# Kernel tuning notes

Hardware: AMD Instinct MI355X
Metric: run time of the kernel (lower is better)

Reference implementation:

```python
import jax, jax.numpy as jnp
from jax import lax
import numpy as np

BINS = 25
K = 5  # entropy patch size
EPS = 1e-5


def conv2d(x, w, b, stride, pad):
    y = lax.conv_general_dilated(x, w, (stride, stride), [(pad, pad), (pad, pad)],
                                 dimension_numbers=("NCHW", "OIHW", "NCHW"))
    return y + b[None, :, None, None]


def group_norm_per_channel(x, w, b):
    # GroupNorm with num_groups == num_channels: per-channel norm over H,W (biased var)
    mu = x.mean(axis=(2, 3), keepdims=True)
    v = x.var(axis=(2, 3), keepdims=True)
    return (x - mu) / jnp.sqrt(v + EPS) * w[None, :, None, None] + b[None, :, None, None]


def channel_entropy(x):
    # x: (b,c,h,w). Unfold into 5x5 patches, per-patch histc(bins=25) over patch
    # values using that patch's min/max range (torch.histc default), then entropy.
    b, c, h, w = x.shape
    ho, wo = h - K + 1, w - K + 1
    # (b,c,K*K,L) -- fixed 25-position loop, vectorized over all data dims
    patches = jnp.stack([x[:, :, i:i + ho, j:j + wo]
                         for i in range(K) for j in range(K)], axis=2)
    patches = patches.reshape(b, c, K * K, ho * wo)
    mn = patches.min(axis=2, keepdims=True)
    mx = patches.max(axis=2, keepdims=True)
    rng = jnp.where(mx > mn, mx - mn, jnp.ones_like(mx))
    bins = jnp.clip(jnp.floor((patches - mn) / rng * BINS), 0, BINS - 1).astype(jnp.int32)
    # histogram via comparison one-hot: (b,c,L,BINS)
    counts = (bins[..., None] == jnp.arange(BINS, dtype=jnp.int32)).sum(axis=2)
    pk = counts.astype(x.dtype) / (K * K)
    ent = (-pk * jnp.log(jnp.clip(pk, 1e-5, 1.0 - 1e-5))).sum(axis=-1).mean(axis=-1)  # (b,c)
    return ent[:, :, None, None]


def instance_norm_ent(x, w, b):
    ent = channel_entropy(lax.stop_gradient(x))
    mu = x.mean(axis=(2, 3), keepdims=True)
    n = x.shape[2] * x.shape[3]
    v = x.var(axis=(2, 3), keepdims=True) * (n / (n - 1))  # unbiased var (torch default)
    return (x - mu) / jnp.sqrt(v + EPS) * w[None, :, None, None] * ent + b[None, :, None, None]


def setup_inputs() -> dict:
    key = jax.random.key(0)
    ks = jax.random.split(key, 24)
    s = 0.05
    d = {
        "x": jax.random.normal(ks[0], (64, 3, 224, 224), jnp.float32),
        "conv0_w": jax.random.normal(ks[1], (8, 3, 7, 7), jnp.float32) * s,
        "conv0_b": jax.random.normal(ks[2], (8,), jnp.float32) * s,
        "conv1_w": jax.random.normal(ks[3], (16, 8, 5, 5), jnp.float32) * s,
        "conv1_b": jax.random.normal(ks[4], (16,), jnp.float32) * s,
        "conv2_w": jax.random.normal(ks[5], (32, 16, 3, 3), jnp.float32) * s,
        "conv2_b": jax.random.normal(ks[6], (32,), jnp.float32) * s,
        "gn0_w": jnp.ones((8,), jnp.float32) + jax.random.normal(ks[7], (8,), jnp.float32) * s,
        "gn0_b": jax.random.normal(ks[8], (8,), jnp.float32) * s,
        "n1_w": jnp.ones((16,), jnp.float32) + jax.random.normal(ks[9], (16,), jnp.float32) * s,
        "n1_b": jax.random.normal(ks[10], (16,), jnp.float32) * s,
        "n2_w": jnp.ones((32,), jnp.float32) + jax.random.normal(ks[11], (32,), jnp.float32) * s,
        "n2_b": jax.random.normal(ks[12], (32,), jnp.float32) * s,
        "bn_g": jnp.ones((10368,), jnp.float32) + jax.random.normal(ks[13], (10368,), jnp.float32) * s,
        "bn_b": jax.random.normal(ks[14], (10368,), jnp.float32) * s,
        "fc1_w": jax.random.normal(ks[15], (32, 10368), jnp.float32) * 0.01,
        "fc1_b": jax.random.normal(ks[16], (32,), jnp.float32) * s,
        "shape_w": jax.random.normal(ks[17], (5, 32), jnp.float32) * s,
        "shape_b": jax.random.normal(ks[18], (5,), jnp.float32) * s,
        "vern_w": jax.random.normal(ks[19], (2, 32), jnp.float32) * s,
        "vern_b": jax.random.normal(ks[20], (2,), jnp.float32) * s,
    }
    return d


def reference(x, conv0_w, conv0_b, conv1_w, conv1_b, conv2_w, conv2_b,
              gn0_w, gn0_b, n1_w, n1_b, n2_w, n2_b,
              bn_g, bn_b, fc1_w, fc1_b, shape_w, shape_b, vern_w, vern_b):
    h = conv2d(x, conv0_w, conv0_b, 4, 2)          # (b,8,56,56)
    h = jax.nn.relu(group_norm_per_channel(h, gn0_w, gn0_b))
    h = conv2d(h, conv1_w, conv1_b, 3, 1)          # (b,16,18,18)
    h = jax.nn.relu(instance_norm_ent(h, n1_w, n1_b))
    h = conv2d(h, conv2_w, conv2_b, 1, 1)          # (b,32,18,18)
    h = jax.nn.relu(instance_norm_ent(h, n2_w, n2_b))
    h = h.reshape(h.shape[0], -1)                  # (b,10368)
    # BatchNorm1d (training mode: batch stats, biased var)
    mu = h.mean(axis=0)
    v = h.var(axis=0)
    h = (h - mu) / jnp.sqrt(v + EPS) * bn_g + bn_b
    h = jax.nn.relu(h @ fc1_w.T + fc1_b)           # (b,32)
    out_shape = jax.nn.softmax(h @ shape_w.T + shape_b, axis=-1)
    out_vern = jax.nn.softmax(h @ vern_w.T + vern_b, axis=-1)
    return (out_shape, out_vern)
```

## Files before the change

kernel.cpp:

```cpp
#include <hip/hip_runtime.h>
#include <math.h>

#define EPSD 1e-5


__device__ __forceinline__ double waveReduceSumD(double v) {
#pragma unroll
    for (int off = 32; off > 0; off >>= 1)
        v += __shfl_down(v, off, 64);
    return v;
}

template <int NW>
__device__ __forceinline__ double blockReduceSumD(double v, double* buf) {
    int lane = threadIdx.x & 63;
    int w = threadIdx.x >> 6;
    v = waveReduceSumD(v);
    __syncthreads();
    if (lane == 0) buf[w] = v;
    __syncthreads();
    double tot = 0.0;
#pragma unroll
    for (int i = 0; i < NW; i++) tot += buf[i];
    return tot;
}

__device__ __forceinline__ void build_ent_tab(float* tab) {
    int t = threadIdx.x;
    if (t < 26) {
        if (t == 0) tab[0] = 0.f;
        else {
            double pk = (double)t / 25.0;
            double cl = fmin(fmax(pk, 1e-5), 1.0 - 1e-5);
            tab[t] = (float)(-pk * log(cl));
        }
    }
}

__device__ __forceinline__ float patch_ent(const float* ch, int py, int px, const float* tab) {
    float pv[25];
#pragma unroll
    for (int i = 0; i < 5; i++)
#pragma unroll
        for (int j = 0; j < 5; j++)
            pv[i * 5 + j] = ch[(py + i) * 18 + px + j];
    float mn = pv[0], mx = pv[0];
#pragma unroll
    for (int k = 1; k < 25; k++) { mn = fminf(mn, pv[k]); mx = fmaxf(mx, pv[k]); }
    float rng = (mx > mn) ? (mx - mn) : 1.0f;
    unsigned long long a0 = 0ull, a1 = 0ull;
    int a2 = 0;
#pragma unroll
    for (int k = 0; k < 25; k++) {
        float tt = (pv[k] - mn) / rng * 25.0f;
        int bi = (int)floorf(tt);
        bi = bi < 0 ? 0 : (bi > 24 ? 24 : bi);
        unsigned sh0 = ((unsigned)(5 * bi)) & 63u;
        unsigned sh1 = ((unsigned)(5 * bi - 60)) & 63u;
        a0 += (bi < 12) ? (1ull << sh0) : 0ull;
        a1 += (bi >= 12 && bi < 24) ? (1ull << sh1) : 0ull;
        a2 += (bi == 24) ? 1 : 0;
    }
    float ent = 0.f;
#pragma unroll
    for (int k = 0; k < 12; k++) ent += tab[(a0 >> (5 * k)) & 31ull];
#pragma unroll
    for (int k = 0; k < 12; k++) ent += tab[(a1 >> (5 * k)) & 31ull];
    ent += tab[a2];
    return ent;
}

__global__ __launch_bounds__(256, 3) void k_conv0(const float* __restrict__ x,
                                                  const float* __restrict__ w,
                                                  const float* __restrict__ bias,
                                                  float* __restrict__ h0raw,
                                                  double* __restrict__ part0) {
    __shared__ float tile[12996];
    __shared__ double redbuf[4][16];
    int tl = blockIdx.x;
    int b = blockIdx.y;
    int t = threadIdx.x;
    for (int i = t; i < 12996; i += 256) tile[i] = 0.f;
    __syncthreads();
    int y_base = tl * 16 - 2;
    const float* xb = x + (size_t)b * 150528;
    for (int i = t; i < 3192; i += 256) {
        int rowid = i / 56, f4 = i % 56;
        int ci = rowid / 19, r = rowid % 19;
        int yIn = y_base + r;
        if (yIn >= 0 && yIn < 224) {
            float4 v = *(const float4*)&xb[ci * 50176 + yIn * 224 + f4 * 4];
            float* tp = tile + ci * 4332 + r * 228;
            tp[114 + f4] = v.x;
            tp[171 + f4] = v.y;
            tp[f4 + 1]   = v.z;
            tp[58 + f4]  = v.w;
        }
    }
    __syncthreads();
    float acc[8];
#pragma unroll
    for (int c = 0; c < 8; c++) acc[c] = 0.f;
    if (t < 224) {
        int ry = t / 56;
        int ox = t % 56;
#pragma unroll
        for (int c = 0; c < 8; c++) acc[c] = bias[c];
#pragma unroll
        for (int ci = 0; ci < 3; ci++) {
#pragma unroll
            for (int ky = 0; ky < 7; ky++) {
                const float* rp = tile + ci * 4332 + (4 * ry + ky) * 228;
#pragma unroll
                for (int kx = 0; kx < 7; kx++) {
                    float v = rp[(kx & 3) * 57 + ox + (kx >> 2)];
#pragma unroll
                    for (int c = 0; c < 8; c++)
                        acc[c] += v * w[c * 147 + ci * 49 + ky * 7 + kx];
                }
            }
        }
        int oy = tl * 4 + ry;
        int opix = oy * 56 + ox;
#pragma unroll
        for (int c = 0; c < 8; c++)
            h0raw[((size_t)b * 8 + c) * 3136 + opix] = acc[c];
    }
    int wv = t >> 6, lane = t & 63;
#pragma unroll
    for (int c = 0; c < 8; c++) {
        double rs = waveReduceSumD((double)acc[c]);
        double rq = waveReduceSumD((double)acc[c] * (double)acc[c]);
        if (lane == 0) { redbuf[wv][c * 2] = rs; redbuf[wv][c * 2 + 1] = rq; }
    }
    __syncthreads();
    if (t < 16) {
        double tot = redbuf[0][t] + redbuf[1][t] + redbuf[2][t] + redbuf[3][t];
        part0[(((size_t)b * 14 + tl) << 4) + t] = tot;
    }
}

__global__ __launch_bounds__(1024) void k_conv1_ent(const float* __restrict__ h0raw,
                                                    const double* __restrict__ part0,
                                                    const float* __restrict__ gw,
                                                    const float* __restrict__ gb,
                                                    const float* __restrict__ w,
                                                    const float* __restrict__ bias,
                                                    const float* __restrict__ nw,
                                                    const float* __restrict__ nb,
                                                    float* __restrict__ h1) {
    __shared__ float xin2[25088];
    __shared__ float vals[1296];
    __shared__ float tab[26];
    __shared__ float gnp[16];
    __shared__ double redbuf[16][2];
    __shared__ double entbuf[16];
    __shared__ float prm[4][3];
    int b = blockIdx.x >> 2;
    int grp = blockIdx.x & 3;
    int t = threadIdx.x;
    if (t < 8) {
        double s = 0.0, s2 = 0.0;
        const double* p = part0 + ((size_t)b * 14) * 16;
        for (int tile = 0; tile < 14; tile++) {
            s += p[tile * 16 + t * 2];
            s2 += p[tile * 16 + t * 2 + 1];
        }
        double mean = s / 3136.0;
        double var = s2 / 3136.0 - mean * mean;
        double rstd = 1.0 / sqrt(var + EPSD);
        double sc = (double)gw[t] * rstd;
        gnp[t] = (float)sc;
        gnp[8 + t] = (float)((double)gb[t] - mean * sc);
    }
    build_ent_tab(tab);
    __syncthreads();
    for (int i = t; i < 25088; i += 1024) {
        int ci = i / 3136, px = i - ci * 3136;
        float v = fmaxf(h0raw[(size_t)b * 25088 + i] * gnp[ci] + gnp[8 + ci], 0.f);
        xin2[(ci >> 1) * 6272 + px * 2 + (ci & 1)] = v;
    }
    __syncthreads();

    int wv = t >> 6, lane = t & 63;
    int c = wv >> 2;
    int q = wv & 3;
    int j_u = __builtin_amdgcn_readfirstlane(grp * 4 + c);
    const float* wg = w + (size_t)j_u * 200;
    float* vch = vals + c * 324;
    float bv = bias[j_u];
    double s = 0.0, s2 = 0.0;
    for (int p = q * 81 + lane; p < q * 81 + 81; p += 64) {
        int oy = p / 18, ox = p - oy * 18;
        int y0 = oy * 3 - 1, x0 = ox * 3 - 1;
        float acc = bv;
        if (oy >= 1 && ox >= 1) {
#pragma unroll
            for (int c2 = 0; c2 < 4; c2++) {
                const float* xp = xin2 + c2 * 6272 + (y0 * 56 + x0) * 2;
                const float* wp0 = wg + (2 * c2) * 25;
#pragma unroll
                for (int ky = 0; ky < 5; ky++)
#pragma unroll
                    for (int kx = 0; kx < 5; kx++) {
                        float2 v = *(const float2*)&xp[(ky * 56 + kx) * 2];
                        acc += v.x * wp0[ky * 5 + kx];
                        acc += v.y * wp0[25 + ky * 5 + kx];
                    }
            }
        } else {
            int ky0 = y0 < 0 ? 1 : 0;
            int kx0 = x0 < 0 ? 1 : 0;
            for (int c2 = 0; c2 < 4; c2++) {
                const float* xp = xin2 + c2 * 6272;
                const float* wp0 = wg + (2 * c2) * 25;
                for (int ky = ky0; ky < 5; ky++) {
                    for (int kx = kx0; kx < 5; kx++) {
                        float2 v = *(const float2*)&xp[((y0 + ky) * 56 + x0 + kx) * 2];
                        acc += v.x * wp0[ky * 5 + kx];
                        acc += v.y * wp0[25 + ky * 5 + kx];
                    }
                }
            }
        }
        vch[p] = acc;
        s += (double)acc; s2 += (double)acc * (double)acc;
    }
    s = waveReduceSumD(s);
    s2 = waveReduceSumD(s2);
    if (lane == 0) { redbuf[wv][0] = s; redbuf[wv][1] = s2; }
    __syncthreads();
    double ent = 0.0;
    if (lane < 49) {
        int pi = q * 49 + lane;
        ent = (double)patch_ent(vch, pi / 14, pi % 14, tab);
    }
    ent = waveReduceSumD(ent);
    if (lane == 0) entbuf[wv] = ent;
    __syncthreads();
    if (t < 4) {
        double ss = 0.0, qq = 0.0, ee = 0.0;
        for (int k = 0; k < 4; k++) {
            ss += redbuf[t * 4 + k][0];
            qq += redbuf[t * 4 + k][1];
            ee += entbuf[t * 4 + k];
        }
        double entmean = ee / 196.0;
        double mean = ss / 324.0;
        double varb = qq / 324.0 - mean * mean;
        double varu = varb * (324.0 / 323.0);
        double rstd = 1.0 / sqrt(varu + EPSD);
        prm[t][0] = (float)mean;
        prm[t][1] = (float)((double)nw[grp * 4 + t] * entmean * rstd);
        prm[t][2] = nb[grp * 4 + t];
    }
    __syncthreads();
    float* outp = h1 + ((size_t)b * 16 + grp * 4) * 324;
    for (int i = t; i < 1296; i += 1024) {
        int cc = i / 324;
        outp[i] = fmaxf((vals[i] - prm[cc][0]) * prm[cc][1] + prm[cc][2], 0.f);
    }
}

__global__ __launch_bounds__(256) void k_conv2_ent(const float* __restrict__ in,
                                                   const float* __restrict__ w,
                                                   const float* __restrict__ bias,
                                                   const float* __restrict__ nw,
                                                   const float* __restrict__ nb,
                                                   float* __restrict__ out) {
    __shared__ float xin[5184];
    __shared__ float vals[324];
    __shared__ float tab[26];
    __shared__ double rbuf[4];
    int b = blockIdx.x >> 5;
    int c = blockIdx.x & 31;
    int t = threadIdx.x;
    const float* xb = in + (size_t)b * 5184;
    for (int i = t; i < 5184; i += 256) xin[i] = xb[i];
    build_ent_tab(tab);
    __syncthreads();
    const float* wc = w + c * 144;
    float bv = bias[c];
    double s = 0.0, s2 = 0.0;
    {
        int oy = 1 + (t >> 4), ox = 1 + (t & 15);
        const float* base = xin + (oy - 1) * 18 + (ox - 1);
        float acc = bv;
#pragma unroll
        for (int ci = 0; ci < 16; ci++) {
            const float* xp = base + ci * 324;
            const float* wp = wc + ci * 9;
#pragma unroll
            for (int ky = 0; ky < 3; ky++)
#pragma unroll
                for (int kx = 0; kx < 3; kx++)
                    acc += xp[ky * 18 + kx] * wp[ky * 3 + kx];
        }
        vals[oy * 18 + ox] = acc;
        s += (double)acc; s2 += (double)acc * (double)acc;
    }
    if (t < 68) {
        int oy, ox;
        if (t < 18)      { oy = 0;      ox = t; }
        else if (t < 36) { oy = 17;     ox = t - 18; }
        else if (t < 52) { oy = t - 35; ox = 0; }
        else             { oy = t - 51; ox = 17; }
        int y0 = oy - 1, x0 = ox - 1;
        int ky0 = y0 < 0 ? 1 : 0;
        int ky1 = (18 - y0) < 3 ? 2 : 3;
        int kx0 = x0 < 0 ? 1 : 0;
        int kx1 = (18 - x0) < 3 ? 2 : 3;
        float acc = bv;
        for (int ci = 0; ci < 16; ci++) {
            const float* xp = xin + ci * 324;
            const float* wp = wc + ci * 9;
            for (int ky = ky0; ky < ky1; ky++) {
                const float* row = xp + (y0 + ky) * 18 + x0;
                for (int kx = kx0; kx < kx1; kx++)
                    acc += row[kx] * wp[ky * 3 + kx];
            }
        }
        vals[oy * 18 + ox] = acc;
        s += (double)acc; s2 += (double)acc * (double)acc;
    }
    __syncthreads();
    double ent = 0.0;
    if (t < 196) ent = (double)patch_ent(vals, t / 14, t % 14, tab);
    double entmean = blockReduceSumD<4>(ent, rbuf) / 196.0;
    double ssum  = blockReduceSumD<4>(s, rbuf);
    double s2sum = blockReduceSumD<4>(s2, rbuf);
    double mean = ssum / 324.0;
    double varb = s2sum / 324.0 - mean * mean;
    double varu = varb * (324.0 / 323.0);
    double rstd = 1.0 / sqrt(varu + EPSD);
    float sc = (float)((double)nw[c] * entmean * rstd);
    float mu = (float)mean;
    float be = nb[c];
    float* outp = out + ((size_t)b * 32 + c) * 324;
    for (int idx = t; idx < 324; idx += 256)
        outp[idx] = fmaxf((vals[idx] - mu) * sc + be, 0.f);
}

__global__ __launch_bounds__(256) void k_bnstats(const float* __restrict__ h2,
                                                 const float* __restrict__ g,
                                                 const float* __restrict__ bb,
                                                 float* __restrict__ scale,
                                                 float* __restrict__ shift) {
    __shared__ double sb[4][64], qb[4][64];
    int lane = threadIdx.x & 63;
    int q = threadIdx.x >> 6;
    int f = blockIdx.x * 64 + lane;
    double s = 0.0, s2 = 0.0;
    for (int b = q * 16; b < q * 16 + 16; b++) {
        double v = (double)h2[(size_t)b * 10368 + f];
        s += v; s2 += v * v;
    }
    sb[q][lane] = s; qb[q][lane] = s2;
    __syncthreads();
    if (threadIdx.x < 64) {
        double S = sb[0][lane] + sb[1][lane] + sb[2][lane] + sb[3][lane];
        double Q = qb[0][lane] + qb[1][lane] + qb[2][lane] + qb[3][lane];
        double mean = S / 64.0;
        double var = Q / 64.0 - mean * mean;
        double rstd = 1.0 / sqrt(var + EPSD);
        double sc = (double)g[f] * rstd;
        scale[f] = (float)sc;
        shift[f] = (float)((double)bb[f] - mean * sc);
    }
}

__global__ __launch_bounds__(256) void k_fc1(const float* __restrict__ h2,
                                             const float* __restrict__ scale,
                                             const float* __restrict__ shift,
                                             const float* __restrict__ w1,
                                             const float* __restrict__ b1,
                                             float* __restrict__ fcout) {
    __shared__ double rbuf[4];
    int b = blockIdx.x >> 5;
    int j = blockIdx.x & 31;
    const float* hb = h2 + (size_t)b * 10368;
    const float* wj = w1 + (size_t)j * 10368;
    double acc = 0.0;
    for (int f = threadIdx.x; f < 10368; f += 256)
        acc += (double)((hb[f] * scale[f] + shift[f]) * wj[f]);
    acc = blockReduceSumD<4>(acc, rbuf);
    if (threadIdx.x == 0)
        fcout[b * 32 + j] = (float)fmax(acc + (double)b1[j], 0.0);
}

__global__ __launch_bounds__(64) void k_heads(const float* __restrict__ fc,
                                              const float* __restrict__ sw,
                                              const float* __restrict__ sb,
                                              const float* __restrict__ vw,
                                              const float* __restrict__ vb,
                                              float* __restrict__ out) {
    int b = threadIdx.x;
    double h[32];
#pragma unroll
    for (int i = 0; i < 32; i++) h[i] = (double)fc[b * 32 + i];
    double lg[5];
    double mx = -1e300;
#pragma unroll
    for (int k = 0; k < 5; k++) {
        double a = (double)sb[k];
#pragma unroll
        for (int i = 0; i < 32; i++) a += h[i] * (double)sw[k * 32 + i];
        lg[k] = a;
        mx = fmax(mx, a);
    }
    double se = 0.0;
#pragma unroll
    for (int k = 0; k < 5; k++) { lg[k] = exp(lg[k] - mx); se += lg[k]; }
#pragma unroll
    for (int k = 0; k < 5; k++) out[b * 5 + k] = (float)(lg[k] / se);
    double l0 = (double)vb[0], l1 = (double)vb[1];
#pragma unroll
    for (int i = 0; i < 32; i++) { l0 += h[i] * (double)vw[i]; l1 += h[i] * (double)vw[32 + i]; }
    double m = fmax(l0, l1);
    double e0 = exp(l0 - m), e1 = exp(l1 - m);
    double inv = 1.0 / (e0 + e1);
    out[320 + b * 2 + 0] = (float)(e0 * inv);
    out[320 + b * 2 + 1] = (float)(e1 * inv);
}

extern "C" void kernel_launch(void* const* d_in, const int* in_sizes, int n_in,
                              void* d_out, int out_size, void* d_ws, size_t ws_size,
                              hipStream_t stream) {
    const float* x       = (const float*)d_in[0];
    const float* conv0_w = (const float*)d_in[1];
    const float* conv0_b = (const float*)d_in[2];
    const float* conv1_w = (const float*)d_in[3];
    const float* conv1_b = (const float*)d_in[4];
    const float* conv2_w = (const float*)d_in[5];
    const float* conv2_b = (const float*)d_in[6];
    const float* gn0_w   = (const float*)d_in[7];
    const float* gn0_b   = (const float*)d_in[8];
    const float* n1_w    = (const float*)d_in[9];
    const float* n1_b    = (const float*)d_in[10];
    const float* n2_w    = (const float*)d_in[11];
    const float* n2_b    = (const float*)d_in[12];
    const float* bn_g    = (const float*)d_in[13];
    const float* bn_b    = (const float*)d_in[14];
    const float* fc1_w   = (const float*)d_in[15];
    const float* fc1_b   = (const float*)d_in[16];
    const float* shape_w = (const float*)d_in[17];
    const float* shape_b = (const float*)d_in[18];
    const float* vern_w  = (const float*)d_in[19];
    const float* vern_b  = (const float*)d_in[20];
    float* out = (float*)d_out;

    double* part0 = (double*)d_ws;
    float* fbase   = (float*)(part0 + 14336);
    float* h0raw   = fbase;
    float* h1      = h0raw + 1605632;
    float* h2      = h1 + 331776;
    float* bnscale = h2 + 663552;
    float* bnshift = bnscale + 10368;
    float* fc      = bnshift + 10368;

    k_conv0<<<dim3(14, 64), dim3(256), 0, stream>>>(x, conv0_w, conv0_b, h0raw, part0);
    k_conv1_ent<<<dim3(256), dim3(1024), 0, stream>>>(h0raw, part0, gn0_w, gn0_b,
                                                      conv1_w, conv1_b, n1_w, n1_b, h1);
    k_conv2_ent<<<dim3(2048), dim3(256), 0, stream>>>(h1, conv2_w, conv2_b, n2_w, n2_b, h2);
    k_bnstats<<<dim3(162), dim3(256), 0, stream>>>(h2, bn_g, bn_b, bnscale, bnshift);
    k_fc1<<<dim3(2048), dim3(256), 0, stream>>>(h2, bnscale, bnshift, fc1_w, fc1_b, fc);
    k_heads<<<dim3(1), dim3(64), 0, stream>>>(fc, shape_w, shape_b, vern_w, vern_b, out);
}
```

Before: 249.2 us.

## Stage conv0 input per channel, pair conv2 channels, vectorize fc1 loads

conv0 now stages one input channel at a time into a smaller shared tile, so the shared-memory footprint drops to a third and the launch bound asks for 6 blocks per CU instead of 3, at the cost of extra barriers per channel. conv2 stores input channels interleaved in pairs so each tap reads a float2 from shared memory, halving the number of LDS loads. fc1 switches to float4 global loads. These are three independent memory-access tweaks across different kernels.

```diff
diff --git a/kernel.cpp b/kernel.cpp
--- a/kernel.cpp
+++ b/kernel.cpp
@@ -70,61 +70,62 @@
     return ent;
 }
 
-__global__ __launch_bounds__(256, 3) void k_conv0(const float* __restrict__ x,
+__global__ __launch_bounds__(256, 6) void k_conv0(const float* __restrict__ x,
                                                   const float* __restrict__ w,
                                                   const float* __restrict__ bias,
                                                   float* __restrict__ h0raw,
                                                   double* __restrict__ part0) {
-    __shared__ float tile[12996];
+    __shared__ __align__(16) float tile[4332];
     __shared__ double redbuf[4][16];
     int tl = blockIdx.x;
     int b = blockIdx.y;
     int t = threadIdx.x;
-    for (int i = t; i < 12996; i += 256) tile[i] = 0.f;
-    __syncthreads();
+    for (int i = t; i < 4332; i += 256) tile[i] = 0.f;
     int y_base = tl * 16 - 2;
     const float* xb = x + (size_t)b * 150528;
-    for (int i = t; i < 3192; i += 256) {
-        int rowid = i / 56, f4 = i % 56;
-        int ci = rowid / 19, r = rowid % 19;
-        int yIn = y_base + r;
-        if (yIn >= 0 && yIn < 224) {
-            float4 v = *(const float4*)&xb[ci * 50176 + yIn * 224 + f4 * 4];
-            float* tp = tile + ci * 4332 + r * 228;
-            tp[114 + f4] = v.x;
-            tp[171 + f4] = v.y;
-            tp[f4 + 1]   = v.z;
-            tp[58 + f4]  = v.w;
-        }
-    }
-    __syncthreads();
     float acc[8];
 #pragma unroll
-    for (int c = 0; c < 8; c++) acc[c] = 0.f;
-    if (t < 224) {
-        int ry = t / 56;
-        int ox = t % 56;
-#pragma unroll
-        for (int c = 0; c < 8; c++) acc[c] = bias[c];
-#pragma unroll
-        for (int ci = 0; ci < 3; ci++) {
+    for (int c = 0; c < 8; c++) acc[c] = bias[c];
+    int ry = t / 56, ox = t % 56;
+    for (int ci = 0; ci < 3; ci++) {
+        __syncthreads();
+        for (int i = t; i < 1064; i += 256) {
+            int r = i / 56, f4 = i % 56;
+            int yIn = y_base + r;
+            if (yIn >= 0 && yIn < 224) {
+                float4 v = *(const float4*)&xb[ci * 50176 + yIn * 224 + f4 * 4];
+                float* tp = tile + r * 228;
+                tp[114 + f4] = v.x;
+                tp[171 + f4] = v.y;
+                tp[f4 + 1]   = v.z;
+                tp[58 + f4]  = v.w;
+            }
+        }
+        __syncthreads();
+        if (t < 224) {
+            const float* wci = w + ci * 49;
 #pragma unroll
             for (int ky = 0; ky < 7; ky++) {
-                const float* rp = tile + ci * 4332 + (4 * ry + ky) * 228;
+                const float* rp = tile + (4 * ry + ky) * 228;
 #pragma unroll
                 for (int kx = 0; kx < 7; kx++) {
                     float v = rp[(kx & 3) * 57 + ox + (kx >> 2)];
 #pragma unroll
                     for (int c = 0; c < 8; c++)
-                        acc[c] += v * w[c * 147 + ci * 49 + ky * 7 + kx];
+                        acc[c] += v * wci[c * 147 + ky * 7 + kx];
                 }
             }
         }
+    }
+    if (t < 224) {
         int oy = tl * 4 + ry;
         int opix = oy * 56 + ox;
 #pragma unroll
         for (int c = 0; c < 8; c++)
             h0raw[((size_t)b * 8 + c) * 3136 + opix] = acc[c];
+    } else {
+#pragma unroll
+        for (int c = 0; c < 8; c++) acc[c] = 0.f;
     }
     int wv = t >> 6, lane = t & 63;
 #pragma unroll
@@ -149,7 +150,7 @@
                                                     const float* __restrict__ nw,
                                                     const float* __restrict__ nb,
                                                     float* __restrict__ h1) {
-    __shared__ float xin2[25088];
+    __shared__ __align__(16) float xin2[25088];
     __shared__ float vals[1296];
     __shared__ float tab[26];
     __shared__ float gnp[16];
@@ -268,7 +269,7 @@
                                                    const float* __restrict__ nw,
                                                    const float* __restrict__ nb,
                                                    float* __restrict__ out) {
-    __shared__ float xin[5184];
+    __shared__ __align__(16) float xin2[5184];
     __shared__ float vals[324];
     __shared__ float tab[26];
     __shared__ double rbuf[4];
@@ -276,7 +277,10 @@
     int c = blockIdx.x & 31;
     int t = threadIdx.x;
     const float* xb = in + (size_t)b * 5184;
-    for (int i = t; i < 5184; i += 256) xin[i] = xb[i];
+    for (int i = t; i < 5184; i += 256) {
+        int ci = i / 324, px = i - ci * 324;
+        xin2[(ci >> 1) * 648 + px * 2 + (ci & 1)] = xb[i];
+    }
     build_ent_tab(tab);
     __syncthreads();
     const float* wc = w + c * 144;
@@ -284,17 +288,20 @@
     double s = 0.0, s2 = 0.0;
     {
         int oy = 1 + (t >> 4), ox = 1 + (t & 15);
-        const float* base = xin + (oy - 1) * 18 + (ox - 1);
+        int base = ((oy - 1) * 18 + (ox - 1)) * 2;
         float acc = bv;
 #pragma unroll
-        for (int ci = 0; ci < 16; ci++) {
-            const float* xp = base + ci * 324;
-            const float* wp = wc + ci * 9;
+        for (int c2 = 0; c2 < 8; c2++) {
+            const float* xp = xin2 + c2 * 648 + base;
+            const float* wp = wc + c2 * 18;
 #pragma unroll
             for (int ky = 0; ky < 3; ky++)
 #pragma unroll
-                for (int kx = 0; kx < 3; kx++)
-                    acc += xp[ky * 18 + kx] * wp[ky * 3 + kx];
+                for (int kx = 0; kx < 3; kx++) {
+                    float2 v = *(const float2*)&xp[(ky * 18 + kx) * 2];
+                    acc += v.x * wp[ky * 3 + kx];
+                    acc += v.y * wp[9 + ky * 3 + kx];
+                }
         }
         vals[oy * 18 + ox] = acc;
         s += (double)acc; s2 += (double)acc * (double)acc;
@@ -311,13 +318,15 @@
         int kx0 = x0 < 0 ? 1 : 0;
         int kx1 = (18 - x0) < 3 ? 2 : 3;
         float acc = bv;
-        for (int ci = 0; ci < 16; ci++) {
-            const float* xp = xin + ci * 324;
-            const float* wp = wc + ci * 9;
+        for (int c2 = 0; c2 < 8; c2++) {
+            const float* xp = xin2 + c2 * 648;
+            const float* wp = wc + c2 * 18;
             for (int ky = ky0; ky < ky1; ky++) {
-                const float* row = xp + (y0 + ky) * 18 + x0;
-                for (int kx = kx0; kx < kx1; kx++)
-                    acc += row[kx] * wp[ky * 3 + kx];
+                for (int kx = kx0; kx < kx1; kx++) {
+                    float2 v = *(const float2*)&xp[((y0 + ky) * 18 + x0 + kx) * 2];
+                    acc += v.x * wp[ky * 3 + kx];
+                    acc += v.y * wp[9 + ky * 3 + kx];
+                }
             }
         }
         vals[oy * 18 + ox] = acc;
@@ -381,8 +390,16 @@
     const float* hb = h2 + (size_t)b * 10368;
     const float* wj = w1 + (size_t)j * 10368;
     double acc = 0.0;
-    for (int f = threadIdx.x; f < 10368; f += 256)
-        acc += (double)((hb[f] * scale[f] + shift[f]) * wj[f]);
+    for (int f = threadIdx.x * 4; f < 10368; f += 1024) {
+        float4 h4 = *(const float4*)&hb[f];
+        float4 s4 = *(const float4*)&scale[f];
+        float4 t4 = *(const float4*)&shift[f];
+        float4 w4 = *(const float4*)&wj[f];
+        acc += (double)((h4.x * s4.x + t4.x) * w4.x);
+        acc += (double)((h4.y * s4.y + t4.y) * w4.y);
+        acc += (double)((h4.z * s4.z + t4.z) * w4.z);
+        acc += (double)((h4.w * s4.w + t4.w) * w4.w);
+    }
     acc = blockReduceSumD<4>(acc, rbuf);
     if (threadIdx.x == 0)
         fcout[b * 32 + j] = (float)fmax(acc + (double)b1[j], 0.0);
```

Result: faster. 227.3 us (-8.8%).
